# Performance work log

Measured on AMD Instinct MI355X. Metric: run time of the kernel, lower is better.

The kernel has to match this reference:

```python
import jax, jax.numpy as jnp
import numpy as np

N, E, IN, H, OUT = 100000, 1200000, 128, 64, 2
L = 3          # num GCN layers
EPS = 1e-5     # BatchNorm eps


def setup_inputs() -> dict:
    key = jax.random.key(0)
    ks = jax.random.split(key, 14)
    x = jax.random.normal(ks[0], (N, IN), dtype=jnp.float32)
    edge_index = jax.random.randint(ks[1], (2, E), 0, N, dtype=jnp.int64)
    # GCNConv weights (glorot-ish scale) and biases
    w0 = jax.random.normal(ks[2], (IN, H), dtype=jnp.float32) / np.float32(np.sqrt(IN))
    w1 = jax.random.normal(ks[3], (H, H), dtype=jnp.float32) / np.float32(np.sqrt(H))
    w2 = jax.random.normal(ks[4], (H, H), dtype=jnp.float32) / np.float32(np.sqrt(H))
    biases = jax.random.normal(ks[5], (L, H), dtype=jnp.float32) * 0.01
    # BatchNorm (eval mode): gamma, beta, running mean/var per layer
    gamma = jnp.ones((L, H), jnp.float32) + 0.1 * jax.random.normal(ks[6], (L, H), dtype=jnp.float32)
    beta = 0.1 * jax.random.normal(ks[7], (L, H), dtype=jnp.float32)
    run_mean = 0.1 * jax.random.normal(ks[8], (L, H), dtype=jnp.float32)
    run_var = 0.5 + jax.random.uniform(ks[9], (L, H), dtype=jnp.float32)  # strictly positive
    # classifier
    cls_w = jax.random.normal(ks[10], (H, OUT), dtype=jnp.float32) / np.float32(np.sqrt(H))
    cls_b = jnp.zeros((OUT,), jnp.float32)
    return {"x": x, "edge_index": edge_index, "w0": w0, "w1": w1, "w2": w2,
            "biases": biases, "gamma": gamma, "beta": beta,
            "run_mean": run_mean, "run_var": run_var,
            "cls_w": cls_w, "cls_b": cls_b}


def reference(x, edge_index, w0, w1, w2, biases, gamma, beta, run_mean, run_var, cls_w, cls_b):
    n = x.shape[0]
    loop = jnp.arange(n, dtype=edge_index.dtype)
    row = jnp.concatenate([edge_index[0], loop])  # source (with self-loops)
    col = jnp.concatenate([edge_index[1], loop])  # target (with self-loops)
    # symmetric normalization: D^{-1/2} (A+I) D^{-1/2}, degree on target index
    deg = jax.ops.segment_sum(jnp.ones(row.shape, x.dtype), col, num_segments=n)
    dinv = jnp.where(deg > 0, jax.lax.rsqrt(deg), 0.0)
    norm = dinv[row] * dinv[col]  # [E+N]

    h = x
    for l, w in enumerate((w0, w1, w2)):
        h = h @ w                                                   # [N,H]
        msg = norm[:, None] * h[row]                                # gather + scale [E+N,H]
        h = jax.ops.segment_sum(msg, col, num_segments=n) + biases[l]
        # BatchNorm1d (eval) + ReLU
        scale = gamma[l] * jax.lax.rsqrt(run_var[l] + EPS)
        h = jax.nn.relu((h - run_mean[l]) * scale + beta[l])
        # dropout is identity in eval mode
    return h @ cls_w + cls_b  # [N, OUT]
```

## Files before the change

### kernel.cpp

```cpp
#include <hip/hip_runtime.h>
#include <hip/hip_fp16.h>

#define EPS 1e-5f
#define ABITS 9
#define ACHUNK 4096
#define BCAP 8192
#define BCSR 12288
#define CSHIFT 13
#define NCHUNK 16

typedef _Float16 half8 __attribute__((ext_vector_type(8)));
typedef float floatx4 __attribute__((ext_vector_type(4)));


__global__ __launch_bounds__(256) void bucketA_kernel(const int* __restrict__ ei, int E,
                                                      int* __restrict__ bucket_fill, unsigned* __restrict__ tmp) {
    __shared__ int2 edg[ACHUNK];
    __shared__ int hist[256], lbase[256], lcur[256];
    int t = threadIdx.x;
    hist[t] = 0; lcur[t] = 0;
    __syncthreads();
    int e0 = blockIdx.x * ACHUNK;
    int e1 = e0 + ACHUNK; if (e1 > E) e1 = E;
    int ne = e1 - e0;
    for (int idx = t; idx < ne; idx += 256) {
        int r = ei[e0 + idx], c = ei[E + e0 + idx];
        edg[idx] = make_int2(r, c);
        atomicAdd(&hist[c >> ABITS], 1);
    }
    __syncthreads();
    int h = hist[t];
    if (h) lbase[t] = atomicAdd(&bucket_fill[t], h);
    __syncthreads();
    for (int idx = t; idx < ne; idx += 256) {
        int2 e = edg[idx];
        int b = e.y >> ABITS;
        int l = atomicAdd(&lcur[b], 1);
        tmp[(size_t)b * BCAP + lbase[b] + l] = ((unsigned)(e.y & 511) << 17) | (unsigned)e.x;
    }
}

__global__ __launch_bounds__(256) void bucketB_kernel(const unsigned* __restrict__ tmp,
                                                      const int* __restrict__ bucket_fill,
                                                      int2* __restrict__ rowse, float* __restrict__ dinv,
                                                      int* __restrict__ csr, int* __restrict__ classCnt, int n) {
    __shared__ unsigned edg[BCAP];
    __shared__ int cnt2[512 * NCHUNK];
    __shared__ int ps[256];
    __shared__ int ccnt[16];
    int b = blockIdx.x, t = threadIdx.x;
    int n0 = b << ABITS;
    int cntN = n - n0; if (cntN > 512) cntN = 512;
    int ne = bucket_fill[b]; if (ne > BCAP) ne = BCAP;
    int base = b * BCAP;
    int cbase = b * BCSR;
    if (t < 16) ccnt[t] = 0;
    for (int i = t; i < 512 * NCHUNK; i += 256) cnt2[i] = 0;
    for (int idx = t; idx < ne; idx += 256) edg[idx] = tmp[(size_t)base + idx];
    __syncthreads();
    for (int idx = t; idx < ne; idx += 256) {
        unsigned e = edg[idx];
        int dstOff = e >> 17, src = e & 0x1FFFF;
        atomicAdd(&cnt2[dstOff * NCHUNK + (src >> CSHIFT)], 1);
    }
    __syncthreads();
    int c0 = 0, c1 = 0;
#pragma unroll
    for (int c = 0; c < NCHUNK; ++c) {
        c0 += cnt2[(2 * t) * NCHUNK + c];
        c1 += cnt2[(2 * t + 1) * NCHUNK + c];
    }
    {
        int k0c = (c0 + 7) >> 3; if (k0c > 15) k0c = 15;
        int k1c = (c1 + 7) >> 3; if (k1c > 15) k1c = 15;
        if (2 * t < cntN) atomicAdd(&ccnt[k0c], 1);
        if (2 * t + 1 < cntN) atomicAdd(&ccnt[k1c], 1);
    }
    int p0 = (c0 + 7) & ~7, p1 = (c1 + 7) & ~7;
    int s = p0 + p1;
    ps[t] = s;
    __syncthreads();
    for (int off = 1; off < 256; off <<= 1) {
        int u = (t >= off) ? ps[t - off] : 0;
        __syncthreads();
        ps[t] += u;
        __syncthreads();
    }
    int excl = ps[t] - s;
    int st0 = cbase + excl, st1 = cbase + excl + p0;
    if (2 * t < cntN) {
        rowse[n0 + 2 * t] = make_int2(st0, st0 + c0);
        dinv[n0 + 2 * t] = rsqrtf((float)(c0 + 1));
    }
    if (2 * t + 1 < cntN) {
        rowse[n0 + 2 * t + 1] = make_int2(st1, st1 + c1);
        dinv[n0 + 2 * t + 1] = rsqrtf((float)(c1 + 1));
    }
    if (2 * t < cntN)
        for (int j = c0; j < p0; ++j) csr[st0 + j] = n0 + 2 * t;
    if (2 * t + 1 < cntN)
        for (int j = c1; j < p1; ++j) csr[st1 + j] = n0 + 2 * t + 1;
    int run = st0;
#pragma unroll
    for (int c = 0; c < NCHUNK; ++c) {
        int v = cnt2[(2 * t) * NCHUNK + c];
        cnt2[(2 * t) * NCHUNK + c] = run;
        run += v;
    }
    run = st1;
#pragma unroll
    for (int c = 0; c < NCHUNK; ++c) {
        int v = cnt2[(2 * t + 1) * NCHUNK + c];
        cnt2[(2 * t + 1) * NCHUNK + c] = run;
        run += v;
    }
    __syncthreads();
    for (int idx = t; idx < ne; idx += 256) {
        unsigned e = edg[idx];
        int dstOff = e >> 17, src = e & 0x1FFFF;
        int key = dstOff * NCHUNK + (src >> CSHIFT);
        int pos = atomicAdd(&cnt2[key], 1);
        csr[pos] = src;
    }
    __syncthreads();
    if (t < 16) atomicAdd(&classCnt[t], ccnt[t]);
}

__global__ __launch_bounds__(256) void perm_kernel(const int2* __restrict__ rowse,
                                                   const int* __restrict__ classCnt,
                                                   int* __restrict__ classCur,
                                                   int* __restrict__ perm, int n) {
    __shared__ int lcnt[16], lbase[16], gbase[16];
    int t = threadIdx.x;
    if (t < 16) lcnt[t] = 0;
    __syncthreads();
    int i = blockIdx.x * 256 + t;
    int k = 0, lrank = 0;
    if (i < n) {
        int2 se = rowse[i];
        int deg = se.y - se.x;
        k = (deg + 7) >> 3; if (k > 15) k = 15;
        lrank = atomicAdd(&lcnt[k], 1);
    }
    __syncthreads();
    if (t < 16) {
        lbase[t] = atomicAdd(&classCur[t], lcnt[t]);
        int bsum = 0;
        for (int j = 0; j < t; ++j) bsum += classCnt[j];
        gbase[t] = bsum;
    }
    __syncthreads();
    if (i < n) perm[gbase[k] + lbase[k] + lrank] = i;
}


template <int K, typename TIN>
__global__ __launch_bounds__(256) void gemm_kernel(const TIN* __restrict__ A, const float* __restrict__ W,
                                                   const float* __restrict__ dinv, __half* __restrict__ out, int n) {
    const int KP = K + 8;
    __shared__ _Float16 Ah[64 * (K + 8)];
    __shared__ _Float16 Wt[64 * (K + 8)];
    int tid = threadIdx.x;

    for (int idx = tid; idx < K * 64; idx += 256) {
        int k = idx >> 6, c = idx & 63;
        Wt[c * KP + k] = (_Float16)W[idx];
    }
    int row0 = blockIdx.x * 64;
    const TIN* Ab = A + (size_t)row0 * K;
    int limit = (n - row0) * K; if (limit > 64 * K) limit = 64 * K;

    if constexpr (sizeof(TIN) == 4) {
        for (int f = tid * 4; f < 64 * K; f += 1024) {
            float4 v = make_float4(0.f, 0.f, 0.f, 0.f);
            if (f + 3 < limit) {
                v = *(const float4*)((const float*)Ab + f);
            } else {
                if (f + 0 < limit) v.x = ((const float*)Ab)[f + 0];
                if (f + 1 < limit) v.y = ((const float*)Ab)[f + 1];
                if (f + 2 < limit) v.z = ((const float*)Ab)[f + 2];
            }
            int row = f / K, k = f % K;
            _Float16* dst = Ah + row * KP + k;
            dst[0] = (_Float16)v.x; dst[1] = (_Float16)v.y;
            dst[2] = (_Float16)v.z; dst[3] = (_Float16)v.w;
        }
    } else {
        for (int f = tid * 8; f < 64 * K; f += 2048) {
            uint4 v = make_uint4(0, 0, 0, 0);
            if (f + 7 < limit) {
                v = *(const uint4*)((const __half*)Ab + f);
            } else {
                const __half* hp = (const __half*)Ab;
                __half tmp8[8];
                for (int j = 0; j < 8; ++j) tmp8[j] = (f + j < limit) ? hp[f + j] : __half(0);
                v = *(const uint4*)tmp8;
            }
            int row = f / K, k = f % K;
            *(uint4*)(Ah + row * KP + k) = v;
        }
    }
    __syncthreads();

    int w = tid >> 6, lane = tid & 63;
    int m = lane & 15, quad = lane >> 4;
    const _Float16* Aw = Ah + (size_t)(w * 16 + m) * KP + quad * 8;
    const _Float16* Bw = Wt + (size_t)m * KP + quad * 8;

    floatx4 acc0 = {0.f, 0.f, 0.f, 0.f}, acc1 = acc0, acc2 = acc0, acc3 = acc0;
    for (int k0 = 0; k0 < K; k0 += 32) {
        half8 a  = *(const half8*)(Aw + k0);
        half8 b0 = *(const half8*)(Bw + 0 * 16 * KP + k0);
        half8 b1 = *(const half8*)(Bw + 1 * 16 * KP + k0);
        half8 b2 = *(const half8*)(Bw + 2 * 16 * KP + k0);
        half8 b3 = *(const half8*)(Bw + 3 * 16 * KP + k0);
        acc0 = __builtin_amdgcn_mfma_f32_16x16x32_f16(a, b0, acc0, 0, 0, 0);
        acc1 = __builtin_amdgcn_mfma_f32_16x16x32_f16(a, b1, acc1, 0, 0, 0);
        acc2 = __builtin_amdgcn_mfma_f32_16x16x32_f16(a, b2, acc2, 0, 0, 0);
        acc3 = __builtin_amdgcn_mfma_f32_16x16x32_f16(a, b3, acc3, 0, 0, 0);
    }

    int rbase = row0 + w * 16 + quad * 4;
#pragma unroll
    for (int r = 0; r < 4; ++r) {
        int row = rbase + r;
        if (row < n) {
            float dv = dinv[row];
            __half* o = out + (size_t)row * 64 + m;
            o[0]  = __float2half(acc0[r] * dv);
            o[16] = __float2half(acc1[r] * dv);
            o[32] = __float2half(acc2[r] * dv);
            o[48] = __float2half(acc3[r] * dv);
        }
    }
}


__device__ __forceinline__ void agg_add8(float4& lo, float4& hi, uint4 raw) {
    float2 p0 = __half22float2(*(const __half2*)&raw.x);
    float2 p1 = __half22float2(*(const __half2*)&raw.y);
    float2 p2 = __half22float2(*(const __half2*)&raw.z);
    float2 p3 = __half22float2(*(const __half2*)&raw.w);
    lo.x += p0.x; lo.y += p0.y; lo.z += p1.x; lo.w += p1.y;
    hi.x += p2.x; hi.y += p2.y; hi.z += p3.x; hi.w += p3.y;
}

__device__ __forceinline__ void agg_core(const __half* __restrict__ t, const float* __restrict__ dinv,
                                         const int2* __restrict__ rowse, const int* __restrict__ csr,
                                         const float* __restrict__ bias, const float* __restrict__ gamma,
                                         const float* __restrict__ beta, const float* __restrict__ mean,
                                         const float* __restrict__ var,
                                         int i, int fl, float4& resL, float4& resH, float& di) {
    uint4 self = *(const uint4*)(t + (size_t)i * 64 + fl * 8);

    float4 lo = make_float4(0.f, 0.f, 0.f, 0.f);
    float4 hi = make_float4(0.f, 0.f, 0.f, 0.f);

    int2 se = rowse[i];
    int deg = se.y - se.x;
    int padEnd = se.x + ((deg + 7) & ~7);
    for (int e = se.x; e < padEnd; e += 8) {
        int s0 = csr[e + 0], s1 = csr[e + 1], s2 = csr[e + 2], s3 = csr[e + 3];
        int s4 = csr[e + 4], s5 = csr[e + 5], s6 = csr[e + 6], s7 = csr[e + 7];
        uint4 r0 = *(const uint4*)(t + (size_t)s0 * 64 + fl * 8);
        uint4 r1 = *(const uint4*)(t + (size_t)s1 * 64 + fl * 8);
        uint4 r2 = *(const uint4*)(t + (size_t)s2 * 64 + fl * 8);
        uint4 r3 = *(const uint4*)(t + (size_t)s3 * 64 + fl * 8);
        uint4 r4 = *(const uint4*)(t + (size_t)s4 * 64 + fl * 8);
        uint4 r5 = *(const uint4*)(t + (size_t)s5 * 64 + fl * 8);
        uint4 r6 = *(const uint4*)(t + (size_t)s6 * 64 + fl * 8);
        uint4 r7 = *(const uint4*)(t + (size_t)s7 * 64 + fl * 8);
        agg_add8(lo, hi, r0); agg_add8(lo, hi, r1); agg_add8(lo, hi, r2); agg_add8(lo, hi, r3);
        agg_add8(lo, hi, r4); agg_add8(lo, hi, r5); agg_add8(lo, hi, r6); agg_add8(lo, hi, r7);
    }

    float coef = 1.0f - (float)(padEnd - se.y);
    {
        float2 p0 = __half22float2(*(const __half2*)&self.x);
        float2 p1 = __half22float2(*(const __half2*)&self.y);
        float2 p2 = __half22float2(*(const __half2*)&self.z);
        float2 p3 = __half22float2(*(const __half2*)&self.w);
        lo.x += coef * p0.x; lo.y += coef * p0.y; lo.z += coef * p1.x; lo.w += coef * p1.y;
        hi.x += coef * p2.x; hi.y += coef * p2.y; hi.z += coef * p3.x; hi.w += coef * p3.y;
    }

    di = dinv[i];
    lo.x *= di; lo.y *= di; lo.z *= di; lo.w *= di;
    hi.x *= di; hi.y *= di; hi.z *= di; hi.w *= di;

    float4 bbL = ((const float4*)bias)[2 * fl],  bbH = ((const float4*)bias)[2 * fl + 1];
    float4 ggL = ((const float4*)gamma)[2 * fl], ggH = ((const float4*)gamma)[2 * fl + 1];
    float4 beL = ((const float4*)beta)[2 * fl],  beH = ((const float4*)beta)[2 * fl + 1];
    float4 mmL = ((const float4*)mean)[2 * fl],  mmH = ((const float4*)mean)[2 * fl + 1];
    float4 vvL = ((const float4*)var)[2 * fl],   vvH = ((const float4*)var)[2 * fl + 1];
    resL.x = fmaxf((lo.x + bbL.x - mmL.x) * (ggL.x * rsqrtf(vvL.x + EPS)) + beL.x, 0.f);
    resL.y = fmaxf((lo.y + bbL.y - mmL.y) * (ggL.y * rsqrtf(vvL.y + EPS)) + beL.y, 0.f);
    resL.z = fmaxf((lo.z + bbL.z - mmL.z) * (ggL.z * rsqrtf(vvL.z + EPS)) + beL.z, 0.f);
    resL.w = fmaxf((lo.w + bbL.w - mmL.w) * (ggL.w * rsqrtf(vvL.w + EPS)) + beL.w, 0.f);
    resH.x = fmaxf((hi.x + bbH.x - mmH.x) * (ggH.x * rsqrtf(vvH.x + EPS)) + beH.x, 0.f);
    resH.y = fmaxf((hi.y + bbH.y - mmH.y) * (ggH.y * rsqrtf(vvH.y + EPS)) + beH.y, 0.f);
    resH.z = fmaxf((hi.z + bbH.z - mmH.z) * (ggH.z * rsqrtf(vvH.z + EPS)) + beH.z, 0.f);
    resH.w = fmaxf((hi.w + bbH.w - mmH.w) * (ggH.w * rsqrtf(vvH.w + EPS)) + beH.w, 0.f);
}

__global__ __launch_bounds__(256, 4) void agg_gemm_kernel(
        const __half* __restrict__ t, const float* __restrict__ dinv,
        const int2* __restrict__ rowse, const int* __restrict__ csr,
        const int* __restrict__ perm,
        const float* __restrict__ bias, const float* __restrict__ gamma,
        const float* __restrict__ beta, const float* __restrict__ mean,
        const float* __restrict__ var,
        const float* __restrict__ W,
        __half* __restrict__ tout, int n) {
    const int KP = 72;
    __shared__ _Float16 Ah[32 * 72];
    __shared__ _Float16 Wt[64 * 72];
    __shared__ int   nidS[32];
    __shared__ float dvS[32];

    int tid = threadIdx.x;
    for (int idx = tid; idx < 64 * 64; idx += 256) {
        int k = idx >> 6, c = idx & 63;
        Wt[c * KP + k] = (_Float16)W[idx];
    }

    int wave = tid >> 6, lane = tid & 63;
    int g = lane >> 3, fl = lane & 7;
    int slotInBlk = wave * 8 + g;
    int slot = blockIdx.x * 32 + slotInBlk;
    bool act = slot < n;

    if (act) {
        int i = perm[slot];
        float4 resL, resH; float di;
        agg_core(t, dinv, rowse, csr, bias, gamma, beta, mean, var, i, fl, resL, resH, di);
        __half2 h0 = __floats2half2_rn(resL.x, resL.y);
        __half2 h1 = __floats2half2_rn(resL.z, resL.w);
        __half2 h2 = __floats2half2_rn(resH.x, resH.y);
        __half2 h3 = __floats2half2_rn(resH.z, resH.w);
        uint4 pk;
        pk.x = *(unsigned*)&h0; pk.y = *(unsigned*)&h1;
        pk.z = *(unsigned*)&h2; pk.w = *(unsigned*)&h3;
        *(uint4*)(Ah + slotInBlk * KP + fl * 8) = pk;
        if (fl == 0) { nidS[slotInBlk] = i; dvS[slotInBlk] = di; }
    } else {
        uint4 z = make_uint4(0, 0, 0, 0);
        *(uint4*)(Ah + slotInBlk * KP + fl * 8) = z;
        if (fl == 0) { nidS[slotInBlk] = 0; dvS[slotInBlk] = 0.f; }
    }
    __syncthreads();

    int m = lane & 15, quad = lane >> 4;
    int mrow = (wave & 1) * 16;
    int c0 = (wave >> 1) * 32;
    const _Float16* Aw = Ah + (mrow + m) * KP + quad * 8;
    const _Float16* Bw = Wt + (c0 + m) * KP + quad * 8;

    floatx4 acc0 = {0.f, 0.f, 0.f, 0.f}, acc1 = acc0;
#pragma unroll
    for (int k0 = 0; k0 < 64; k0 += 32) {
        half8 a  = *(const half8*)(Aw + k0);
        half8 b0 = *(const half8*)(Bw + k0);
        half8 b1 = *(const half8*)(Bw + 16 * KP + k0);
        acc0 = __builtin_amdgcn_mfma_f32_16x16x32_f16(a, b0, acc0, 0, 0, 0);
        acc1 = __builtin_amdgcn_mfma_f32_16x16x32_f16(a, b1, acc1, 0, 0, 0);
    }

#pragma unroll
    for (int r = 0; r < 4; ++r) {
        int row = mrow + quad * 4 + r;
        if (blockIdx.x * 32 + row < n) {
            int node = nidS[row];
            float dv = dvS[row];
            __half* o = tout + (size_t)node * 64;
            o[c0 + m]      = __float2half(acc0[r] * dv);
            o[c0 + 16 + m] = __float2half(acc1[r] * dv);
        }
    }
}

__global__ __launch_bounds__(256, 4) void agg_cls_kernel(
        const __half* __restrict__ t, const float* __restrict__ dinv,
        const int2* __restrict__ rowse, const int* __restrict__ csr,
        const int* __restrict__ perm,
        const float* __restrict__ bias, const float* __restrict__ gamma,
        const float* __restrict__ beta, const float* __restrict__ mean,
        const float* __restrict__ var,
        float* __restrict__ fout,
        const float* __restrict__ cls_w, const float* __restrict__ cls_b,
        int n) {
    int wave = threadIdx.x >> 6;
    int lane = threadIdx.x & 63;
    int g = lane >> 3;
    int fl = lane & 7;
    int slot = (blockIdx.x * (blockDim.x >> 6) + wave) * 8 + g;
    if (slot >= n) return;
    int i = perm[slot];

    float4 resL, resH; float di;
    agg_core(t, dinv, rowse, csr, bias, gamma, beta, mean, var, i, fl, resL, resH, di);

    const float4* cw = (const float4*)cls_w;
    float4 cwA = cw[4 * fl + 0], cwB = cw[4 * fl + 1], cwC = cw[4 * fl + 2], cwD = cw[4 * fl + 3];
    float c0 = resL.x * cwA.x + resL.y * cwA.z + resL.z * cwB.x + resL.w * cwB.z
             + resH.x * cwC.x + resH.y * cwC.z + resH.z * cwD.x + resH.w * cwD.z;
    float c1 = resL.x * cwA.y + resL.y * cwA.w + resL.z * cwB.y + resL.w * cwB.w
             + resH.x * cwC.y + resH.y * cwC.w + resH.z * cwD.y + resH.w * cwD.w;
    for (int off = 4; off > 0; off >>= 1) {
        c0 += __shfl_xor(c0, off);
        c1 += __shfl_xor(c1, off);
    }
    if (fl == 0) {
        fout[(size_t)i * 2 + 0] = c0 + cls_b[0];
        fout[(size_t)i * 2 + 1] = c1 + cls_b[1];
    }
}


extern "C" void kernel_launch(void* const* d_in, const int* in_sizes, int n_in,
                              void* d_out, int out_size, void* d_ws, size_t ws_size,
                              hipStream_t stream) {
    const float* x      = (const float*)d_in[0];
    const int*   ei     = (const int*)d_in[1];
    const float* w0     = (const float*)d_in[2];
    const float* w1     = (const float*)d_in[3];
    const float* w2     = (const float*)d_in[4];
    const float* biases = (const float*)d_in[5];
    const float* gamma  = (const float*)d_in[6];
    const float* beta   = (const float*)d_in[7];
    const float* rmean  = (const float*)d_in[8];
    const float* rvar   = (const float*)d_in[9];
    const float* cls_w  = (const float*)d_in[10];
    const float* cls_b  = (const float*)d_in[11];
    float* out = (float*)d_out;

    const int IN = 128, H = 64;
    const int N = in_sizes[0] / IN;
    const int E = in_sizes[1] / 2;

    char* p = (char*)d_ws;
    auto carve = [&](size_t bytes) { void* q = (void*)p; p += (bytes + 255) & ~(size_t)255; return q; };
    float* dinv    = (float*)carve((size_t)N * 4);
    int2*  rowse   = (int2*)carve((size_t)N * 8);
    int*   meta    = (int*)carve((size_t)288 * 4);
    int*   perm    = (int*)carve((size_t)N * 4);
    unsigned* tmp  = (unsigned*)carve((size_t)256 * BCAP * 4);
    int*   csr     = (int*)carve((size_t)256 * BCSR * 4);
    __half* tA     = (__half*)carve((size_t)N * H * 2);
    __half* tB     = (__half*)carve((size_t)N * H * 2);

    int* bucket_fill = meta;
    int* classCnt    = meta + 256;
    int* classCur    = meta + 272;

    int nbuckets = (N + (1 << ABITS) - 1) >> ABITS;
    int na = (E + ACHUNK - 1) / ACHUNK;

    hipMemsetAsync(meta, 0, (size_t)288 * 4, stream);
    bucketA_kernel<<<na, 256, 0, stream>>>(ei, E, bucket_fill, tmp);
    bucketB_kernel<<<nbuckets, 256, 0, stream>>>(tmp, bucket_fill, rowse, dinv, csr, classCnt, N);
    perm_kernel<<<(N + 255) / 256, 256, 0, stream>>>(rowse, classCnt, classCur, perm, N);

    int gemm_grid = (N + 63) / 64;
    int agg_grid  = (N + 31) / 32;

    gemm_kernel<128, float><<<gemm_grid, 256, 0, stream>>>(x, w0, dinv, tA, N);
    agg_gemm_kernel<<<agg_grid, 256, 0, stream>>>(tA, dinv, rowse, csr, perm,
        biases + 0, gamma + 0, beta + 0, rmean + 0, rvar + 0, w1, tB, N);
    agg_gemm_kernel<<<agg_grid, 256, 0, stream>>>(tB, dinv, rowse, csr, perm,
        biases + H, gamma + H, beta + H, rmean + H, rvar + H, w2, tA, N);
    agg_cls_kernel<<<agg_grid, 256, 0, stream>>>(tA, dinv, rowse, csr, perm,
        biases + 2 * H, gamma + 2 * H, beta + 2 * H, rmean + 2 * H, rvar + 2 * H,
        out, cls_w, cls_b, N);
}
```

Baseline: 243.0 us.

## Fold degree-class permutation into bucketB and stage agg_gemm output through LDS

New measurement: 251.5 us. +3.5%, slower.

```diff
diff --git a/kernel.cpp b/kernel.cpp
--- a/kernel.cpp
+++ b/kernel.cpp
@@ -43,11 +43,11 @@
 __global__ __launch_bounds__(256) void bucketB_kernel(const unsigned* __restrict__ tmp,
                                                       const int* __restrict__ bucket_fill,
                                                       int2* __restrict__ rowse, float* __restrict__ dinv,
-                                                      int* __restrict__ csr, int* __restrict__ classCnt, int n) {
+                                                      int* __restrict__ csr, int* __restrict__ perm, int n) {
     __shared__ unsigned edg[BCAP];
     __shared__ int cnt2[512 * NCHUNK];
     __shared__ int ps[256];
-    __shared__ int ccnt[16];
+    __shared__ int ccnt[16], cbaseS[16];
     int b = blockIdx.x, t = threadIdx.x;
     int n0 = b << ABITS;
     int cntN = n - n0; if (cntN > 512) cntN = 512;
@@ -70,12 +70,11 @@
         c0 += cnt2[(2 * t) * NCHUNK + c];
         c1 += cnt2[(2 * t + 1) * NCHUNK + c];
     }
-    {
-        int k0c = (c0 + 7) >> 3; if (k0c > 15) k0c = 15;
-        int k1c = (c1 + 7) >> 3; if (k1c > 15) k1c = 15;
-        if (2 * t < cntN) atomicAdd(&ccnt[k0c], 1);
-        if (2 * t + 1 < cntN) atomicAdd(&ccnt[k1c], 1);
-    }
+    int k0c = (c0 + 7) >> 3; if (k0c > 15) k0c = 15;
+    int k1c = (c1 + 7) >> 3; if (k1c > 15) k1c = 15;
+    int rank0 = 0, rank1 = 0;
+    if (2 * t < cntN)     rank0 = atomicAdd(&ccnt[k0c], 1);
+    if (2 * t + 1 < cntN) rank1 = atomicAdd(&ccnt[k1c], 1);
     int p0 = (c0 + 7) & ~7, p1 = (c1 + 7) & ~7;
     int s = p0 + p1;
     ps[t] = s;
@@ -114,7 +113,14 @@
         cnt2[(2 * t + 1) * NCHUNK + c] = run;
         run += v;
     }
-    __syncthreads();
+    if (t < 16) {
+        int sacc = 0;
+        for (int j = 0; j < t; ++j) sacc += ccnt[j];
+        cbaseS[t] = sacc;
+    }
+    __syncthreads();
+    if (2 * t < cntN)     perm[n0 + cbaseS[k0c] + rank0] = n0 + 2 * t;
+    if (2 * t + 1 < cntN) perm[n0 + cbaseS[k1c] + rank1] = n0 + 2 * t + 1;
     for (int idx = t; idx < ne; idx += 256) {
         unsigned e = edg[idx];
         int dstOff = e >> 17, src = e & 0x1FFFF;
@@ -122,35 +128,6 @@
         int pos = atomicAdd(&cnt2[key], 1);
         csr[pos] = src;
     }
-    __syncthreads();
-    if (t < 16) atomicAdd(&classCnt[t], ccnt[t]);
-}
-
-__global__ __launch_bounds__(256) void perm_kernel(const int2* __restrict__ rowse,
-                                                   const int* __restrict__ classCnt,
-                                                   int* __restrict__ classCur,
-                                                   int* __restrict__ perm, int n) {
-    __shared__ int lcnt[16], lbase[16], gbase[16];
-    int t = threadIdx.x;
-    if (t < 16) lcnt[t] = 0;
-    __syncthreads();
-    int i = blockIdx.x * 256 + t;
-    int k = 0, lrank = 0;
-    if (i < n) {
-        int2 se = rowse[i];
-        int deg = se.y - se.x;
-        k = (deg + 7) >> 3; if (k > 15) k = 15;
-        lrank = atomicAdd(&lcnt[k], 1);
-    }
-    __syncthreads();
-    if (t < 16) {
-        lbase[t] = atomicAdd(&classCur[t], lcnt[t]);
-        int bsum = 0;
-        for (int j = 0; j < t; ++j) bsum += classCnt[j];
-        gbase[t] = bsum;
-    }
-    __syncthreads();
-    if (i < n) perm[gbase[k] + lbase[k] + lrank] = i;
 }
 
 
@@ -365,17 +342,21 @@
         acc0 = __builtin_amdgcn_mfma_f32_16x16x32_f16(a, b0, acc0, 0, 0, 0);
         acc1 = __builtin_amdgcn_mfma_f32_16x16x32_f16(a, b1, acc1, 0, 0, 0);
     }
+    __syncthreads();
 
 #pragma unroll
     for (int r = 0; r < 4; ++r) {
         int row = mrow + quad * 4 + r;
-        if (blockIdx.x * 32 + row < n) {
-            int node = nidS[row];
-            float dv = dvS[row];
-            __half* o = tout + (size_t)node * 64;
-            o[c0 + m]      = __float2half(acc0[r] * dv);
-            o[c0 + 16 + m] = __float2half(acc1[r] * dv);
-        }
+        float dv = dvS[row];
+        Ah[row * KP + c0 + m]      = (_Float16)(acc0[r] * dv);
+        Ah[row * KP + c0 + 16 + m] = (_Float16)(acc1[r] * dv);
+    }
+    __syncthreads();
+
+    if (act) {
+        int node = nidS[slotInBlk];
+        uint4 v = *(const uint4*)(Ah + slotInBlk * KP + fl * 8);
+        *(uint4*)(tout + (size_t)node * 64 + fl * 8) = v;
     }
 }
 
@@ -442,24 +423,19 @@
     auto carve = [&](size_t bytes) { void* q = (void*)p; p += (bytes + 255) & ~(size_t)255; return q; };
     float* dinv    = (float*)carve((size_t)N * 4);
     int2*  rowse   = (int2*)carve((size_t)N * 8);
-    int*   meta    = (int*)carve((size_t)288 * 4);
+    int*   bucket_fill = (int*)carve((size_t)256 * 4);
     int*   perm    = (int*)carve((size_t)N * 4);
     unsigned* tmp  = (unsigned*)carve((size_t)256 * BCAP * 4);
     int*   csr     = (int*)carve((size_t)256 * BCSR * 4);
     __half* tA     = (__half*)carve((size_t)N * H * 2);
     __half* tB     = (__half*)carve((size_t)N * H * 2);
 
-    int* bucket_fill = meta;
-    int* classCnt    = meta + 256;
-    int* classCur    = meta + 272;
-
     int nbuckets = (N + (1 << ABITS) - 1) >> ABITS;
     int na = (E + ACHUNK - 1) / ACHUNK;
 
-    hipMemsetAsync(meta, 0, (size_t)288 * 4, stream);
+    hipMemsetAsync(bucket_fill, 0, (size_t)256 * 4, stream);
     bucketA_kernel<<<na, 256, 0, stream>>>(ei, E, bucket_fill, tmp);
-    bucketB_kernel<<<nbuckets, 256, 0, stream>>>(tmp, bucket_fill, rowse, dinv, csr, classCnt, N);
-    perm_kernel<<<(N + 255) / 256, 256, 0, stream>>>(rowse, classCnt, classCur, perm, N);
+    bucketB_kernel<<<nbuckets, 256, 0, stream>>>(tmp, bucket_fill, rowse, dinv, csr, perm, N);
 
     int gemm_grid = (N + 63) / 64;
     int agg_grid  = (N + 31) / 32;
```
